# Optimization experiments

Hardware: AMD Instinct MI355X
Metric: run time of the kernel (lower is better)

The kernel has to match this reference:

```python
import jax, jax.numpy as jnp
import numpy as np

N_NODES = 50000


def _gine_conv(x, src, dst, edge_attr, ew, eb, w1, b1, w2, b2, eps=0.0):
    # message: ReLU(x_j + Linear(edge_attr))  -- PyG GINEConv with edge_dim lin
    m = jax.nn.relu(x[src] + edge_attr @ ew + eb)          # [E, D]
    agg = jax.ops.segment_sum(m, dst, num_segments=N_NODES)  # [N, D]
    h = (1.0 + eps) * x + agg
    # nn: Linear -> ReLU -> Linear
    return jax.nn.relu(h @ w1 + b1) @ w2 + b2


def setup_inputs() -> dict:
    key = jax.random.key(0)
    ks = jax.random.split(key, 16)
    Cin, H, Cout, Ed = 128, 256, 256, 16
    E = 800000
    x = jax.random.normal(ks[0], (N_NODES, Cin), dtype=jnp.float32)
    edge_index = jax.random.randint(ks[1], (2, E), 0, N_NODES, dtype=jnp.int32)
    edge_attr = jax.random.normal(ks[2], (E, Ed), dtype=jnp.float32)

    def lin(k, fan_in, fan_out):
        s = 1.0 / np.sqrt(fan_in)
        kw, kb = jax.random.split(k)
        w = jax.random.uniform(kw, (fan_in, fan_out), minval=-s, maxval=s, dtype=jnp.float32)
        b = jax.random.uniform(kb, (fan_out,), minval=-s, maxval=s, dtype=jnp.float32)
        return w, b

    e1_w, e1_b = lin(ks[3], Ed, Cin)     # conv1 edge lin: edge_dim -> in_channels
    l11_w, l11_b = lin(ks[4], Cin, H)    # conv1 MLP layer 1
    l12_w, l12_b = lin(ks[5], H, Cout)   # conv1 MLP layer 2
    e2_w, e2_b = lin(ks[6], Ed, H)       # conv2 edge lin: edge_dim -> hidden
    l21_w, l21_b = lin(ks[7], H, H)      # conv2 MLP layer 1
    l22_w, l22_b = lin(ks[8], H, Cout)   # conv2 MLP layer 2
    return {
        "x": x, "edge_index": edge_index, "edge_attr": edge_attr,
        "e1_w": e1_w, "e1_b": e1_b, "l11_w": l11_w, "l11_b": l11_b,
        "l12_w": l12_w, "l12_b": l12_b,
        "e2_w": e2_w, "e2_b": e2_b, "l21_w": l21_w, "l21_b": l21_b,
        "l22_w": l22_w, "l22_b": l22_b,
    }


def reference(x, edge_index, edge_attr,
              e1_w, e1_b, l11_w, l11_b, l12_w, l12_b,
              e2_w, e2_b, l21_w, l21_b, l22_w, l22_b):
    src, dst = edge_index[0], edge_index[1]
    h = _gine_conv(x, src, dst, edge_attr, e1_w, e1_b, l11_w, l11_b, l12_w, l12_b)
    h = _gine_conv(h, src, dst, edge_attr, e2_w, e2_b, l21_w, l21_b, l22_w, l22_b)
    return h
```

## Files before the change

kernel.cpp:

```cpp
#include <hip/hip_runtime.h>
#include <type_traits>

#define N_NODES 50000

using short8  = __attribute__((ext_vector_type(8))) short;
using floatx4 = __attribute__((ext_vector_type(4))) float;
using f32x2   = __attribute__((ext_vector_type(2))) float;

__device__ inline unsigned short f2b(float f) {
    unsigned u = __float_as_uint(f);
    u += 0x7FFFu + ((u >> 16) & 1u);
    return (unsigned short)(u >> 16);
}
__device__ inline float b2f(unsigned short h) {
    return __uint_as_float(((unsigned)h) << 16);
}

__device__ inline f32x2 pk_fma_lo(f32x2 a, f32x2 b, f32x2 c) {
    f32x2 d;
    asm("v_pk_fma_f32 %0, %1, %2, %3 op_sel_hi:[0,1,1]"
        : "=v"(d) : "v"(a), "v"(b), "v"(c));
    return d;
}
__device__ inline f32x2 pk_fma_hi(f32x2 a, f32x2 b, f32x2 c) {
    f32x2 d;
    asm("v_pk_fma_f32 %0, %1, %2, %3 op_sel:[1,0,0] op_sel_hi:[1,1,1]"
        : "=v"(d) : "v"(a), "v"(b), "v"(c));
    return d;
}
__device__ inline f32x2 pk_add(f32x2 a, f32x2 b) {
    f32x2 d;
    asm("v_pk_add_f32 %0, %1, %2" : "=v"(d) : "v"(a), "v"(b));
    return d;
}

__global__ __launch_bounds__(256) void zero_int_kernel(int* __restrict__ p, int n)
{
    int i = blockIdx.x * 256 + threadIdx.x;
    if (i < n) p[i] = 0;
}

__global__ __launch_bounds__(256) void hist_kernel(const int* __restrict__ dstv,
                                                   int* __restrict__ cnt, int E)
{
    int e = blockIdx.x * 256 + threadIdx.x;
    if (e < E) atomicAdd(&cnt[dstv[e]], 1);
}

__global__ __launch_bounds__(256) void scanA_kernel(const int* __restrict__ cnt,
                                                    int* __restrict__ row_start,
                                                    int* __restrict__ bsum, int n)
{
    __shared__ int s[256];
    int t = threadIdx.x;
    int i = blockIdx.x * 256 + t;
    int val = (i < n) ? cnt[i] : 0;
    s[t] = val;
    __syncthreads();
#pragma unroll
    for (int off = 1; off < 256; off <<= 1) {
        int v = (t >= off) ? s[t - off] : 0;
        __syncthreads();
        s[t] += v;
        __syncthreads();
    }
    if (i < n) row_start[i] = s[t] - val;
    if (t == 255) bsum[blockIdx.x] = s[255];
}

__global__ __launch_bounds__(256) void scanB_kernel(int* __restrict__ bsum, int nb)
{
    __shared__ int s[256];
    int t = threadIdx.x;
    int val = (t < nb) ? bsum[t] : 0;
    s[t] = val;
    __syncthreads();
#pragma unroll
    for (int off = 1; off < 256; off <<= 1) {
        int v = (t >= off) ? s[t - off] : 0;
        __syncthreads();
        s[t] += v;
        __syncthreads();
    }
    if (t < nb) bsum[t] = s[t] - val;
}

__global__ __launch_bounds__(256) void scanC_kernel(int* __restrict__ row_start,
                                                    int* __restrict__ woff,
                                                    const int* __restrict__ bsum, int n)
{
    int i = blockIdx.x * 256 + threadIdx.x;
    if (i < n) {
        int v = row_start[i] + bsum[blockIdx.x];
        row_start[i] = v;
        woff[i] = v;
    }
}

__global__ __launch_bounds__(256) void scatter_kernel(const int* __restrict__ srcv,
                                                      const int* __restrict__ dstv,
                                                      int* __restrict__ woff,
                                                      int2* __restrict__ sorted2, int E)
{
    int e = blockIdx.x * 256 + threadIdx.x;
    if (e < E) {
        int pos = atomicAdd(&woff[dstv[e]], 1);
        sorted2[pos] = make_int2(srcv[e], e);
    }
}

__global__ __launch_bounds__(256) void castT_kernel(const float* __restrict__ w,
                                                    unsigned short* __restrict__ out, int K)
{
    int i = blockIdx.x * 256 + threadIdx.x;
    if (i < K * 256) {
        int k = i >> 8, c = i & 255;
        out[c * K + k] = f2b(w[i]);
    }
}

template<int D, bool XB>
__global__ __launch_bounds__(256, (D == 256) ? 3 : 4) void agg_kernel(
    const float*          __restrict__ xf,
    const unsigned short* __restrict__ xb,
    const float*          __restrict__ ea,
    const float*          __restrict__ ew,
    const float*          __restrict__ ebias,
    const int*            __restrict__ row_start,
    const int*            __restrict__ cnt,
    const int2*           __restrict__ sorted2,
    float*                __restrict__ agg,
    int N)
{
    constexpr int DPL = D / 64;
    constexpr int NP  = DPL / 2;
    using XT = std::conditional_t<XB, ushort4,
               std::conditional_t<DPL == 2, float2, float4>>;

    __shared__ float sEA[4][2][64][16];

    const int lane = threadIdx.x & 63;
    const int w    = threadIdx.x >> 6;
    const int W    = gridDim.x * 4;
    int node = blockIdx.x * 4 + w;
    const int d0 = lane * DPL;
    if (node >= N) return;

    f32x2 wrp[16 * NP];
#pragma unroll
    for (int k = 0; k < 16; ++k) {
        if constexpr (NP == 1) {
            float2 w2 = *reinterpret_cast<const float2*>(ew + k * D + d0);
            wrp[k] = f32x2{w2.x, w2.y};
        } else {
            float4 w4 = *reinterpret_cast<const float4*>(ew + k * D + d0);
            wrp[k * 2 + 0] = f32x2{w4.x, w4.y};
            wrp[k * 2 + 1] = f32x2{w4.z, w4.w};
        }
    }
    f32x2 bx[NP];
#pragma unroll
    for (int p = 0; p < NP; ++p)
        bx[p] = f32x2{ebias[d0 + 2 * p], ebias[d0 + 2 * p + 1]};

    f32x2 acc[NP];

    auto STAGE = [&](int2 prv, int cb, int bi) {
        const int sweeps = (cb + 15) >> 4;
        const int chunk  = lane & 3;
        const int sl0    = lane >> 2;
        for (int j = 0; j < sweeps; ++j) {
            int sl  = j * 16 + sl0;
            int eid = __shfl(prv.y, sl);
            if (sl >= cb) eid = 0;
            const float* gp = ea + (size_t)eid * 16 + chunk * 4;
            __builtin_amdgcn_global_load_lds(gp, &sEA[w][bi][j * 16][0], 16, 0, 0);
        }
    };

    auto COMPUTE = [&](const float4& E0, const float4& E1,
                       const float4& E2, const float4& E3, const XT& X) {
        f32x2 ap[8] = {f32x2{E0.x, E0.y}, f32x2{E0.z, E0.w},
                       f32x2{E1.x, E1.y}, f32x2{E1.z, E1.w},
                       f32x2{E2.x, E2.y}, f32x2{E2.z, E2.w},
                       f32x2{E3.x, E3.y}, f32x2{E3.z, E3.w}};
        f32x2 m[NP];
        if constexpr (XB) {
            m[0] = pk_add(bx[0], f32x2{b2f(X.x), b2f(X.y)});
            m[1] = pk_add(bx[1], f32x2{b2f(X.z), b2f(X.w)});
        } else if constexpr (NP == 1) {
            m[0] = pk_add(bx[0], f32x2{X.x, X.y});
        } else {
            m[0] = pk_add(bx[0], f32x2{X.x, X.y});
            m[1] = pk_add(bx[1], f32x2{X.z, X.w});
        }
#pragma unroll
        for (int kp = 0; kp < 8; ++kp) {
#pragma unroll
            for (int p = 0; p < NP; ++p)
                m[p] = pk_fma_lo(ap[kp], wrp[(2 * kp) * NP + p], m[p]);
#pragma unroll
            for (int p = 0; p < NP; ++p)
                m[p] = pk_fma_hi(ap[kp], wrp[(2 * kp + 1) * NP + p], m[p]);
        }
#pragma unroll
        for (int p = 0; p < NP; ++p) {
            f32x2 r{fmaxf(m[p].x, 0.f), fmaxf(m[p].y, 0.f)};
            acc[p] = pk_add(acc[p], r);
        }
    };

    auto RUN = [&](int cb, int bi, int2 prv) {
        if (cb <= 0) return;
        float4 EA0, EA1, EA2, EA3, EB0, EB1, EB2, EB3;
        XT xA, xB;
        auto LA = [&](int i) {
            const float4* rp = reinterpret_cast<const float4*>(&sEA[w][bi][i][0]);
            EA0 = rp[0]; EA1 = rp[1]; EA2 = rp[2]; EA3 = rp[3];
            int s = __builtin_amdgcn_readlane(prv.x, i);
            if constexpr (XB) xA = *reinterpret_cast<const XT*>(xb + (size_t)s * D + d0);
            else              xA = *reinterpret_cast<const XT*>(xf + (size_t)s * D + d0);
        };
        auto LB = [&](int i) {
            const float4* rp = reinterpret_cast<const float4*>(&sEA[w][bi][i][0]);
            EB0 = rp[0]; EB1 = rp[1]; EB2 = rp[2]; EB3 = rp[3];
            int s = __builtin_amdgcn_readlane(prv.x, i);
            if constexpr (XB) xB = *reinterpret_cast<const XT*>(xb + (size_t)s * D + d0);
            else              xB = *reinterpret_cast<const XT*>(xf + (size_t)s * D + d0);
        };
        LA(0);
        int i = 0;
        while (true) {
            if (i + 1 < cb) LB(i + 1);
            COMPUTE(EA0, EA1, EA2, EA3, xA);
            ++i; if (i >= cb) break;
            if (i + 1 < cb) LA(i + 1);
            COMPUTE(EB0, EB1, EB2, EB3, xB);
            ++i; if (i >= cb) break;
        }
    };

    int s0 = __builtin_amdgcn_readfirstlane(row_start[node]);
    int c  = __builtin_amdgcn_readfirstlane(cnt[node]);
    int cb = min(c, 64);
    int2 pr = make_int2(0, 0);
    if (lane < cb) pr = sorted2[s0 + lane];
    STAGE(pr, cb, 0);
    int buf = 0;

    int nnode = node + W;
    int ns0 = 0, nc = 0;
    if (nnode < N) { ns0 = row_start[nnode]; nc = cnt[nnode]; }

    asm volatile("s_waitcnt vmcnt(0)" ::: "memory");

    while (true) {
        int  ncb = 0;
        int2 npr = make_int2(0, 0);
        if (nnode < N) {
            ns0 = __builtin_amdgcn_readfirstlane(ns0);
            nc  = __builtin_amdgcn_readfirstlane(nc);
            ncb = min(nc, 64);
            if (lane < ncb) npr = sorted2[ns0 + lane];
        }
        int nnnode = nnode + W;
        int nns0 = 0, nnc = 0;
        if (nnnode < N) { nns0 = row_start[nnnode]; nnc = cnt[nnnode]; }

#pragma unroll
        for (int p = 0; p < NP; ++p) acc[p] = f32x2{0.f, 0.f};

        RUN(cb, buf, pr);

        for (int base = 64; base < c; base += 64) {
            int cb2 = min(64, c - base);
            int2 pv = make_int2(0, 0);
            if (lane < cb2) pv = sorted2[s0 + base + lane];
            STAGE(pv, cb2, buf);
            asm volatile("s_waitcnt vmcnt(0)" ::: "memory");
            RUN(cb2, buf, pv);
        }

        if constexpr (NP == 1)
            *reinterpret_cast<float2*>(agg + (size_t)node * D + d0) =
                make_float2(acc[0].x, acc[0].y);
        else
            *reinterpret_cast<float4*>(agg + (size_t)node * D + d0) =
                make_float4(acc[0].x, acc[0].y, acc[1].x, acc[1].y);

        if (nnode >= N) break;
        STAGE(npr, ncb, buf ^ 1);
        asm volatile("s_waitcnt vmcnt(0)" ::: "memory");

        node = nnode; s0 = ns0; c = nc; cb = ncb; pr = npr; buf ^= 1;
        nnode = nnnode; ns0 = nns0; nc = nnc;
    }
}

template<int DIN, bool L1>
__global__ __launch_bounds__(256) void node_mfma_kernel(
    const float*          __restrict__ basef,
    const unsigned short* __restrict__ baseb,
    const float*          __restrict__ agg,
    const unsigned short* __restrict__ w1T,
    const float*          __restrict__ b1,
    const unsigned short* __restrict__ w2T,
    const float*          __restrict__ b2,
    unsigned short*       __restrict__ outb,
    float*                __restrict__ outf,
    int N)
{
    __shared__ unsigned short hs[64 * DIN];
    __shared__ unsigned short ts[64 * 256];
    const int tid = threadIdx.x;
    const int n0 = blockIdx.x * 64;

#pragma unroll
    for (int it = 0; it < (64 * DIN) / (256 * 8); ++it) {
        int flat = (it * 256 + tid) * 8;
        int r = flat / DIN, c = flat % DIN;
        int node = n0 + r;
        float v[8];
        if (node < N) {
            const float* ap = agg + (size_t)node * DIN + c;
            float4 a0 = *reinterpret_cast<const float4*>(ap);
            float4 a1 = *reinterpret_cast<const float4*>(ap + 4);
            float a[8] = {a0.x, a0.y, a0.z, a0.w, a1.x, a1.y, a1.z, a1.w};
            if constexpr (L1) {
                const float* bp = basef + (size_t)node * DIN + c;
                float4 x0 = *reinterpret_cast<const float4*>(bp);
                float4 x1 = *reinterpret_cast<const float4*>(bp + 4);
                float xx[8] = {x0.x, x0.y, x0.z, x0.w, x1.x, x1.y, x1.z, x1.w};
#pragma unroll
                for (int j = 0; j < 8; ++j) v[j] = a[j] + xx[j];
            } else {
                short8 xv = *reinterpret_cast<const short8*>(baseb + (size_t)node * DIN + c);
#pragma unroll
                for (int j = 0; j < 8; ++j) v[j] = a[j] + b2f((unsigned short)xv[j]);
            }
        } else {
#pragma unroll
            for (int j = 0; j < 8; ++j) v[j] = 0.f;
        }
        short8 o;
#pragma unroll
        for (int j = 0; j < 8; ++j) o[j] = (short)f2b(v[j]);
        *reinterpret_cast<short8*>(&hs[r * DIN + (c ^ ((r & 7) << 3))]) = o;
    }
    __syncthreads();

    const int wv = tid >> 6, lane = tid & 63;
    const int lr = lane & 15, lk = (lane >> 4) * 8;
    const int colbase = wv * 64;

    floatx4 acc[4][4];
#pragma unroll
    for (int n = 0; n < 4; ++n) {
        float bn = b1[colbase + n * 16 + lr];
#pragma unroll
        for (int m = 0; m < 4; ++m) acc[m][n] = floatx4{bn, bn, bn, bn};
    }
#pragma unroll
    for (int kk = 0; kk < DIN; kk += 32) {
        short8 af[4], bf[4];
#pragma unroll
        for (int m = 0; m < 4; ++m) {
            int row = m * 16 + lr;
            af[m] = *reinterpret_cast<const short8*>(
                &hs[row * DIN + ((kk + lk) ^ ((row & 7) << 3))]);
        }
#pragma unroll
        for (int n = 0; n < 4; ++n) {
            int col = colbase + n * 16 + lr;
            bf[n] = *reinterpret_cast<const short8*>(w1T + (size_t)col * DIN + kk + lk);
        }
#pragma unroll
        for (int m = 0; m < 4; ++m)
#pragma unroll
            for (int n = 0; n < 4; ++n)
                acc[m][n] = __builtin_amdgcn_mfma_f32_16x16x32_bf16(af[m], bf[n], acc[m][n], 0, 0, 0);
    }
#pragma unroll
    for (int m = 0; m < 4; ++m)
#pragma unroll
        for (int n = 0; n < 4; ++n)
#pragma unroll
            for (int r = 0; r < 4; ++r) {
                int row = m * 16 + (lane >> 4) * 4 + r;
                int col = colbase + n * 16 + lr;
                ts[row * 256 + (col ^ ((row & 7) << 3))] = f2b(fmaxf(acc[m][n][r], 0.f));
            }
    __syncthreads();

    floatx4 acc2[4][4];
#pragma unroll
    for (int n = 0; n < 4; ++n) {
        float bn = b2[colbase + n * 16 + lr];
#pragma unroll
        for (int m = 0; m < 4; ++m) acc2[m][n] = floatx4{bn, bn, bn, bn};
    }
#pragma unroll
    for (int kk = 0; kk < 256; kk += 32) {
        short8 af[4], bf[4];
#pragma unroll
        for (int m = 0; m < 4; ++m) {
            int row = m * 16 + lr;
            af[m] = *reinterpret_cast<const short8*>(
                &ts[row * 256 + ((kk + lk) ^ ((row & 7) << 3))]);
        }
#pragma unroll
        for (int n = 0; n < 4; ++n) {
            int col = colbase + n * 16 + lr;
            bf[n] = *reinterpret_cast<const short8*>(w2T + (size_t)col * 256 + kk + lk);
        }
#pragma unroll
        for (int m = 0; m < 4; ++m)
#pragma unroll
            for (int n = 0; n < 4; ++n)
                acc2[m][n] = __builtin_amdgcn_mfma_f32_16x16x32_bf16(af[m], bf[n], acc2[m][n], 0, 0, 0);
    }
#pragma unroll
    for (int m = 0; m < 4; ++m)
#pragma unroll
        for (int n = 0; n < 4; ++n)
#pragma unroll
            for (int r = 0; r < 4; ++r) {
                int row = m * 16 + (lane >> 4) * 4 + r;
                int node = n0 + row;
                int col = colbase + n * 16 + lr;
                if (node < N) {
                    if constexpr (L1) outb[(size_t)node * 256 + col] = f2b(acc2[m][n][r]);
                    else              outf[(size_t)node * 256 + col] = acc2[m][n][r];
                }
            }
}

extern "C" void kernel_launch(void* const* d_in, const int* in_sizes, int n_in,
                              void* d_out, int out_size, void* d_ws, size_t ws_size,
                              hipStream_t stream)
{
    const float* x    = (const float*)d_in[0];
    const int*   ei   = (const int*)  d_in[1];
    const float* ea   = (const float*)d_in[2];
    const float* e1w  = (const float*)d_in[3];
    const float* e1b  = (const float*)d_in[4];
    const float* w11  = (const float*)d_in[5];
    const float* b11  = (const float*)d_in[6];
    const float* w12  = (const float*)d_in[7];
    const float* b12  = (const float*)d_in[8];
    const float* e2w  = (const float*)d_in[9];
    const float* e2b  = (const float*)d_in[10];
    const float* w21  = (const float*)d_in[11];
    const float* b21  = (const float*)d_in[12];
    const float* w22  = (const float*)d_in[13];
    const float* b22  = (const float*)d_in[14];

    const int E = in_sizes[1] / 2;
    const int N = N_NODES;
    const int* src = ei;
    const int* dst = ei + E;

    char* cur = (char*)d_ws;
    float* aggb = (float*)cur;            cur += (size_t)N * 256 * 4;
    int*   cnt       = (int*)cur;         cur += (size_t)N * 4;
    int*   row_start = (int*)cur;         cur += (size_t)N * 4;
    int*   woff      = (int*)cur;         cur += (size_t)N * 4;
    int*   bsum      = (int*)cur;         cur += 256 * 4;
    int2*  sorted2   = (int2*)cur;        cur += (size_t)E * 8;
    unsigned short* h1b  = (unsigned short*)cur; cur += (size_t)N * 256 * 2;
    unsigned short* w11T = (unsigned short*)cur; cur += 128 * 256 * 2;
    unsigned short* w12T = (unsigned short*)cur; cur += 256 * 256 * 2;
    unsigned short* w21T = (unsigned short*)cur; cur += 256 * 256 * 2;
    unsigned short* w22T = (unsigned short*)cur; cur += 256 * 256 * 2;
    float* outp = (float*)d_out;

    const int nbN = (N + 255) / 256;
    const int nbE = (E + 255) / 256;

    castT_kernel<<<(128 * 256 + 255) / 256, 256, 0, stream>>>(w11, w11T, 128);
    castT_kernel<<<256, 256, 0, stream>>>(w12, w12T, 256);
    castT_kernel<<<256, 256, 0, stream>>>(w21, w21T, 256);
    castT_kernel<<<256, 256, 0, stream>>>(w22, w22T, 256);

    zero_int_kernel<<<nbN, 256, 0, stream>>>(cnt, N);
    hist_kernel<<<nbE, 256, 0, stream>>>(dst, cnt, E);
    scanA_kernel<<<nbN, 256, 0, stream>>>(cnt, row_start, bsum, N);
    scanB_kernel<<<1, 256, 0, stream>>>(bsum, nbN);
    scanC_kernel<<<nbN, 256, 0, stream>>>(row_start, woff, bsum, N);
    scatter_kernel<<<nbE, 256, 0, stream>>>(src, dst, woff, sorted2, E);

    const int nbNode = (N + 63) / 64;

    agg_kernel<128, false><<<1024, 256, 0, stream>>>(
        x, nullptr, ea, e1w, e1b, row_start, cnt, sorted2, aggb, N);
    node_mfma_kernel<128, true><<<nbNode, 256, 0, stream>>>(
        x, nullptr, aggb, w11T, b11, w12T, b12, h1b, nullptr, N);

    agg_kernel<256, true><<<768, 256, 0, stream>>>(
        nullptr, h1b, ea, e2w, e2b, row_start, cnt, sorted2, aggb, N);
    node_mfma_kernel<256, false><<<nbNode, 256, 0, stream>>>(
        nullptr, h1b, aggb, w21T, b21, w22T, b22, nullptr, outp, N);
}
```

Baseline: 476.3 us.

## Replace persistent grid-stride aggregation with one-wave-per-node launch

The aggregation kernel no longer runs as a persistent grid (1024/768 blocks) that loops over nodes with cross-node prefetch of CSR metadata and edge attributes. Instead it launches one wavefront per node, and prefetching is limited to the next 64-edge chunk inside that node. The occupancy hint is also removed from launch bounds. This drops the cross-node software pipeline and its register cost in favour of hardware wave scheduling. In exchange, every wave reloads the edge-linear weights and bias, and latency hiding between nodes now depends on occupancy.

```diff
diff --git a/kernel.cpp b/kernel.cpp
--- a/kernel.cpp
+++ b/kernel.cpp
@@ -120,7 +120,7 @@
 }
 
 template<int D, bool XB>
-__global__ __launch_bounds__(256, (D == 256) ? 3 : 4) void agg_kernel(
+__global__ __launch_bounds__(256) void agg_kernel(
     const float*          __restrict__ xf,
     const unsigned short* __restrict__ xb,
     const float*          __restrict__ ea,
@@ -141,10 +141,9 @@
 
     const int lane = threadIdx.x & 63;
     const int w    = threadIdx.x >> 6;
-    const int W    = gridDim.x * 4;
-    int node = blockIdx.x * 4 + w;
+    const int node = blockIdx.x * 4 + w;
+    if (node >= N) return;
     const int d0 = lane * DPL;
-    if (node >= N) return;
 
     f32x2 wrp[16 * NP];
 #pragma unroll
@@ -161,19 +160,22 @@
     f32x2 bx[NP];
 #pragma unroll
     for (int p = 0; p < NP; ++p)
-        bx[p] = f32x2{ebias[d0 + 2 * p], ebias[d0 + 2 * p + 1]};
+        bx[p] = f32x2{ebias[d0 + p * 2], ebias[d0 + p * 2 + 1]};
 
     f32x2 acc[NP];
+#pragma unroll
+    for (int p = 0; p < NP; ++p) acc[p] = f32x2{0.f, 0.f};
+
+    const int s0 = __builtin_amdgcn_readfirstlane(row_start[node]);
+    const int c  = __builtin_amdgcn_readfirstlane(cnt[node]);
 
     auto STAGE = [&](int2 prv, int cb, int bi) {
         const int sweeps = (cb + 15) >> 4;
-        const int chunk  = lane & 3;
-        const int sl0    = lane >> 2;
         for (int j = 0; j < sweeps; ++j) {
-            int sl  = j * 16 + sl0;
+            int sl  = j * 16 + (lane >> 2);
             int eid = __shfl(prv.y, sl);
             if (sl >= cb) eid = 0;
-            const float* gp = ea + (size_t)eid * 16 + chunk * 4;
+            const float* gp = ea + (size_t)eid * 16 + (lane & 3) * 4;
             __builtin_amdgcn_global_load_lds(gp, &sEA[w][bi][j * 16][0], 16, 0, 0);
         }
     };
@@ -240,61 +242,35 @@
         }
     };
 
-    int s0 = __builtin_amdgcn_readfirstlane(row_start[node]);
-    int c  = __builtin_amdgcn_readfirstlane(cnt[node]);
-    int cb = min(c, 64);
+    int cb0 = min(c, 64);
     int2 pr = make_int2(0, 0);
-    if (lane < cb) pr = sorted2[s0 + lane];
-    STAGE(pr, cb, 0);
-    int buf = 0;
-
-    int nnode = node + W;
-    int ns0 = 0, nc = 0;
-    if (nnode < N) { ns0 = row_start[nnode]; nc = cnt[nnode]; }
-
+    if (lane < cb0) pr = sorted2[s0 + lane];
+    STAGE(pr, cb0, 0);
     asm volatile("s_waitcnt vmcnt(0)" ::: "memory");
 
+    int buf = 0, base = 0;
     while (true) {
-        int  ncb = 0;
-        int2 npr = make_int2(0, 0);
-        if (nnode < N) {
-            ns0 = __builtin_amdgcn_readfirstlane(ns0);
-            nc  = __builtin_amdgcn_readfirstlane(nc);
-            ncb = min(nc, 64);
-            if (lane < ncb) npr = sorted2[ns0 + lane];
-        }
-        int nnnode = nnode + W;
-        int nns0 = 0, nnc = 0;
-        if (nnnode < N) { nns0 = row_start[nnnode]; nnc = cnt[nnnode]; }
-
-#pragma unroll
-        for (int p = 0; p < NP; ++p) acc[p] = f32x2{0.f, 0.f};
-
-        RUN(cb, buf, pr);
-
-        for (int base = 64; base < c; base += 64) {
-            int cb2 = min(64, c - base);
-            int2 pv = make_int2(0, 0);
-            if (lane < cb2) pv = sorted2[s0 + base + lane];
-            STAGE(pv, cb2, buf);
-            asm volatile("s_waitcnt vmcnt(0)" ::: "memory");
-            RUN(cb2, buf, pv);
-        }
-
-        if constexpr (NP == 1)
-            *reinterpret_cast<float2*>(agg + (size_t)node * D + d0) =
-                make_float2(acc[0].x, acc[0].y);
-        else
-            *reinterpret_cast<float4*>(agg + (size_t)node * D + d0) =
-                make_float4(acc[0].x, acc[0].y, acc[1].x, acc[1].y);
-
-        if (nnode >= N) break;
-        STAGE(npr, ncb, buf ^ 1);
+        const int cc = min(64, c - base);
+        const int nbase = base + 64;
+        int2 prn = make_int2(0, 0);
+        int ccn = 0;
+        if (nbase < c) {
+            ccn = min(64, c - nbase);
+            if (lane < ccn) prn = sorted2[s0 + nbase + lane];
+            STAGE(prn, ccn, buf ^ 1);
+        }
+        RUN(cc, buf, pr);
+        if (nbase >= c) break;
         asm volatile("s_waitcnt vmcnt(0)" ::: "memory");
-
-        node = nnode; s0 = ns0; c = nc; cb = ncb; pr = npr; buf ^= 1;
-        nnode = nnnode; ns0 = nns0; nc = nnc;
-    }
+        pr = prn; base = nbase; buf ^= 1;
+    }
+
+    if constexpr (NP == 1)
+        *reinterpret_cast<float2*>(agg + (size_t)node * D + d0) =
+            make_float2(acc[0].x, acc[0].y);
+    else
+        *reinterpret_cast<float4*>(agg + (size_t)node * D + d0) =
+            make_float4(acc[0].x, acc[0].y, acc[1].x, acc[1].y);
 }
 
 template<int DIN, bool L1>
@@ -489,14 +465,15 @@
     scanC_kernel<<<nbN, 256, 0, stream>>>(row_start, woff, bsum, N);
     scatter_kernel<<<nbE, 256, 0, stream>>>(src, dst, woff, sorted2, E);
 
+    const int nbAgg  = (N + 3) / 4;
     const int nbNode = (N + 63) / 64;
 
-    agg_kernel<128, false><<<1024, 256, 0, stream>>>(
+    agg_kernel<128, false><<<nbAgg, 256, 0, stream>>>(
         x, nullptr, ea, e1w, e1b, row_start, cnt, sorted2, aggb, N);
     node_mfma_kernel<128, true><<<nbNode, 256, 0, stream>>>(
         x, nullptr, aggb, w11T, b11, w12T, b12, h1b, nullptr, N);
 
-    agg_kernel<256, true><<<768, 256, 0, stream>>>(
+    agg_kernel<256, true><<<nbAgg, 256, 0, stream>>>(
         nullptr, h1b, ea, e2w, e2b, row_start, cnt, sorted2, aggb, N);
     node_mfma_kernel<256, false><<<nbNode, 256, 0, stream>>>(
         nullptr, h1b, aggb, w21T, b21, w22T, b22, nullptr, outp, N);
```

Result: slower. 516.2 us (+8.4%).
